# Kernel tuning notes

Hardware: AMD Instinct MI355X
Metric: run time of the kernel (lower is better)

## Reference

```python
import jax, jax.numpy as jnp
import numpy as np

K = 24          # SiFinder.KERNEL_SIZE
SIGMA = 1e-6    # SiFinder.CORR_SIGMA


def setup_inputs() -> dict:
    key = jax.random.key(0)
    k1, k2, k3 = jax.random.split(key, 3)
    H = W = 480
    x_dec = jax.random.normal(k1, (1, 3, H, W), dtype=jnp.float32)
    y_dec = jax.random.normal(k2, (1, 3, H, W), dtype=jnp.float32)
    y = jax.random.normal(k3, (1, 3, H, W), dtype=jnp.float32)
    return {"x_dec": x_dec, "y_dec": y_dec, "y": y}


def _get_x_patches(x_dec):
    # non-overlapping KxK patches, raster order (rows of patches, then cols)
    _, C, H, W = x_dec.shape
    p = x_dec[0].reshape(C, H // K, K, W // K, K)
    return p.transpose(1, 3, 0, 2, 4).reshape(-1, C, K, K)  # (P, C, K, K)


def _conv(img, w):
    # valid cross-correlation, matches F.conv2d
    return jax.lax.conv_general_dilated(
        img, w, window_strides=(1, 1), padding='VALID',
        dimension_numbers=('NCHW', 'OIHW', 'NCHW'))


def _pearson_corr(x_patches, y):
    C = x_patches.shape[1]
    ps = C * K * K  # patch_size
    mean_x = jnp.mean(x_patches, axis=(1, 2, 3))[None, :, None, None]   # (1,P,1,1)
    sum_x2 = jnp.sum(x_patches ** 2, axis=(1, 2, 3))[None, :, None, None]
    ones = jnp.ones((1, C, K, K), y.dtype)
    sum_y = _conv(y, ones)            # (1,1,H',W'); torch builds P identical channels
    xy = _conv(y, x_patches)          # (1,P,H',W')
    numer = xy / ps - mean_x * sum_y / ps
    den_x = sum_x2 / ps - mean_x ** 2
    den_y = _conv(y ** 2, ones) / ps - sum_y ** 2 / ps ** 2
    return (2 * numer + SIGMA) / (jnp.abs(den_x) + jnp.abs(den_y) + SIGMA)


def _forward(x_dec, y_dec, y):
    x_patches = _get_x_patches(x_dec)
    corr = _pearson_corr(x_patches, y_dec)          # (1, P, H', W')
    _, P, Hc, Wc = corr.shape
    idx = jnp.argmax(corr[0].reshape(P, Hc * Wc), axis=-1)
    rows, cols = idx // Wc, idx % Wc
    # roi_align(boxes=[-0.5+c, -0.5+r, ...], out=KxK, sampling_ratio=-1) samples
    # exactly at integer pixel centers -> reduces to an exact patch gather from y.
    C = y.shape[1]
    def take(r, c):
        return jax.lax.dynamic_slice(y[0], (0, r, c), (C, K, K))
    patches = jax.vmap(take)(rows, cols)            # (P, C, K, K)
    # nn.Fold with stride==kernel: stitch non-overlapping patches back to image
    H, W = x_dec.shape[2], x_dec.shape[3]
    img = patches.reshape(H // K, W // K, C, K, K).transpose(2, 0, 3, 1, 4)
    return img.reshape(1, C, H, W)


def reference(x_dec, y_dec, y):
    return _forward(x_dec, y_dec, y)
```

## Files before the change

### kernel.cpp

```cpp
#include <hip/hip_runtime.h>
#include <stdint.h>

#define HW    480
#define KS    24
#define CH    3
#define HO    457
#define NPOS  (HO*HO)
#define NP    400
#define PS    (CH*KS*KS)
#define SIG   1e-6f
#define NSQ   54
#define NMT   13
#define NIY   115
#define NGRP  (NIY*8*4)
#define MAXF  16384
#define RGRID 4096
#define DELTA 4e-3f
#define QS    28.0f
#define IS2   (1.0f/(QS*QS))
#define PB    2608

typedef __attribute__((ext_vector_type(4)))  int  int4v;
typedef __attribute__((ext_vector_type(16))) int  int16v;
typedef unsigned int uint;
typedef unsigned char uchar;
typedef unsigned long long ull;

static __device__ __forceinline__ char q8(float v) {
    float s = rintf(v * QS);
    s = fminf(127.f, fmaxf(-127.f, s));
    return (char)(int)s;
}
static __device__ __forceinline__ uint mono(float f) {
    uint u = __float_as_uint(f);
    return (u & 0x80000000u) ? ~u : (u | 0x80000000u);
}
static __device__ __forceinline__ float unmono(uint u) {
    uint b = (u & 0x80000000u) ? (u & 0x7fffffffu) : ~u;
    return __uint_as_float(b);
}

__global__ void fat1_k(const float* __restrict__ x, const float* __restrict__ yd,
                       float* __restrict__ Wp, char* __restrict__ yq,
                       float* __restrict__ cs, float* __restrict__ cs2) {
    int b = blockIdx.x;
    if (b < 2700) {
        int t = b * 256 + threadIdx.x;
        int p = t / PS, e = t - p * PS;
        int c = e / (KS * KS);
        int r = (e / KS) % KS;
        int w = e % KS;
        int pr = p / 20, pc = p - pr * 20;
        Wp[t] = x[c * HW * HW + (pr * KS + r) * HW + (pc * KS + w)];
    } else if (b < 5400) {
        int t = (b - 2700) * 256 + threadIdx.x;
        yq[t] = q8(yd[t]);
    } else {
        int t = (b - 5400) * 256 + threadIdx.x;
        if (t >= HO * HW) return;
        int i = t / HW, w = t - i * HW;
        float s = 0.f, s2 = 0.f;
        for (int c = 0; c < CH; c++) {
            const float* base = yd + c * HW * HW + i * HW + w;
            for (int dh = 0; dh < KS; dh++) {
                float v = base[dh * HW];
                s += v; s2 += v * v;
            }
        }
        cs[t] = s; cs2[t] = s2;
    }
}

__global__ void fat2_k(const float* __restrict__ Wp,
                       const float* __restrict__ cs, const float* __restrict__ cs2,
                       float* __restrict__ meanX, float* __restrict__ denXa,
                       char* __restrict__ Aq,
                       float* __restrict__ sumY, float* __restrict__ denYa,
                       uint* __restrict__ cnt, ull* __restrict__ best) {
    __shared__ float shs[4], shs2[4];
    int b = blockIdx.x;
    if (b < 400) {
        int p = b;
        if (threadIdx.x == 1) best[p] = 0ull;
        if (b == 0 && threadIdx.x == 2) *cnt = 0u;
        float s = 0.f, s2 = 0.f;
        for (int e = threadIdx.x; e < PS; e += 256) {
            float v = Wp[p * PS + e];
            s += v; s2 += v * v;
        }
        for (int o = 32; o > 0; o >>= 1) { s += __shfl_down(s, o); s2 += __shfl_down(s2, o); }
        int lane = threadIdx.x & 63, wv = threadIdx.x >> 6;
        if (lane == 0) { shs[wv] = s; shs2[wv] = s2; }
        __syncthreads();
        if (threadIdx.x == 0) {
            float S = shs[0] + shs[1] + shs[2] + shs[3];
            float S2 = shs2[0] + shs2[1] + shs2[2] + shs2[3];
            float m = S / (float)PS;
            meanX[p] = m;
            denXa[p] = fabsf(S2 / (float)PS - m * m);
        }
    } else if (b < 3208) {
        int id = (b - 400) * 256 + threadIdx.x;
        int e    = id & 15;
        int lane = (id >> 4) & 63;
        int f    = id >> 10;
        int s    = f % NSQ;
        int mtg  = f / NSQ;
        int kk = s * 32 + (lane >> 5) * 16 + e;
        int p  = mtg * 32 + (lane & 31);
        float v = (p < NP) ? Wp[p * PS + kk] : 0.f;
        Aq[id] = q8(v);
    } else {
        int t = (b - 3208) * 256 + threadIdx.x;
        if (t >= NPOS) return;
        int i = t / HO, j = t - i * HO;
        const float* r  = cs  + i * HW + j;
        const float* r2 = cs2 + i * HW + j;
        float s = 0.f, s2 = 0.f;
        for (int d = 0; d < KS; d++) { s += r[d]; s2 += r2[d]; }
        sumY[t] = s;
        float ips = 1.0f / (float)PS;
        denYa[t] = fabsf(s2 * ips - (s * ips) * (s * ips));
    }
}

static __device__ __forceinline__ void stage_c(uchar* __restrict__ S,
                                               const char* __restrict__ yq,
                                               int c, int i0, int j0, int tid) {
    for (int it = tid; it < 27 * 6; it += 256) {
        int row = it / 6;
        int gb  = (it - row * 6) * 16;
        int yr  = i0 + row;
        int gj  = j0 + gb;
        uint d[6];
        if (yr < HW && gj + 24 <= HW) {
            const uchar* src = (const uchar*)yq + ((size_t)(c * HW + yr)) * HW + gj;
            uint4 a = *(const uint4*)src;
            uint2 bb = *(const uint2*)(src + 16);
            d[0] = a.x; d[1] = a.y; d[2] = a.z; d[3] = a.w; d[4] = bb.x; d[5] = bb.y;
        } else {
            uchar tmp[24];
#pragma unroll
            for (int e = 0; e < 24; e++) {
                int col = gj + e;
                tmp[e] = (yr < HW && col < HW)
                       ? ((const uchar*)yq)[((size_t)(c * HW + yr)) * HW + col] : (uchar)0;
            }
            const uint* tp = (const uint*)tmp;
#pragma unroll
            for (int e = 0; e < 6; e++) d[e] = tp[e];
        }
        int base = row * 96 + gb;
#pragma unroll
        for (int pi = 0; pi < 8; pi++) {
            const int a = pi >> 2;
            const int r = pi & 3;
            uint4 w;
            if (r == 0)
                w = make_uint4(d[a], d[a + 1], d[a + 2], d[a + 3]);
            else
                w = make_uint4((d[a]     >> (8 * r)) | (d[a + 1] << (32 - 8 * r)),
                               (d[a + 1] >> (8 * r)) | (d[a + 2] << (32 - 8 * r)),
                               (d[a + 2] >> (8 * r)) | (d[a + 3] << (32 - 8 * r)),
                               (d[a + 3] >> (8 * r)) | (d[a + 4] << (32 - 8 * r)));
            *(uint4*)&S[pi * PB + base] = w;
        }
    }
}

template<int MT>
static __device__ __forceinline__ void corr1_body(
        const int mt0,
        const char* __restrict__ yq, const char* __restrict__ Aq,
        const float* __restrict__ meanX, const float* __restrict__ denXa,
        const float* __restrict__ sumY, const float* __restrict__ denYa,
        uint* __restrict__ table, uchar* __restrict__ S) {
    const int tid  = threadIdx.x;
    const int lane = tid & 63;
    const int g    = tid >> 6;
    const int n    = lane & 31;
    const int kha  = lane >> 5;
    const int jx   = blockIdx.x;
    const int iy   = blockIdx.y;
    const int j0   = 64 * jx;
    const int i0   = 4 * iy;
    const int i    = i0 + g;

    const int olo[3] = { kha ? 16  : 0,   kha ? 192 : 104, kha ? 296 : 208 };
    const int ohi[3] = { kha ? 96  : 8,   kha ? 200 : 112, kha ? 304 : 288 };

    const uchar* Bt0g = S + ((2 * n) & 7) * PB + ((2 * n) & ~7) + g * 96;
    const uchar* Bt1g = Bt0g + PB;

    const char* Ab0 = Aq + ((size_t)mt0 * NSQ << 10) + lane * 16;
    const char* Ab[2] = { Ab0, Ab0 + ((size_t)NSQ << 10) };

    int16v acc[MT][2];
#pragma unroll
    for (int mt = 0; mt < MT; mt++)
#pragma unroll
        for (int t = 0; t < 2; t++) acc[mt][t] = (int16v)0;

    int4v av[2][MT][3];
#pragma unroll
    for (int mt = 0; mt < MT; mt++)
#pragma unroll
        for (int u = 0; u < 3; u++)
            av[0][mt][u] = *(const int4v*)(Ab[mt] + (u << 10));

#pragma unroll
    for (int c = 0; c < CH; c++) {
        __syncthreads();
        stage_c(S, yq, c, i0, j0, tid);
        __syncthreads();

#pragma unroll
        for (int q = 0; q < 6; q++) {
            const int Q   = c * 6 + q;
            const int cur = Q & 1;
            if (Q < 17) {
#pragma unroll
                for (int mt = 0; mt < MT; mt++)
#pragma unroll
                    for (int u = 0; u < 3; u++)
                        av[cur ^ 1][mt][u] =
                            *(const int4v*)(Ab[mt] + (((Q + 1) * 3 + u) << 10));
            }
            const uchar* Bq0 = Bt0g + 384 * q;
            const uchar* Bq1 = Bt1g + 384 * q;
            uint2 blo[3][2], bhi[3][2];
#pragma unroll
            for (int u = 0; u < 3; u++) {
                blo[u][0] = *(const uint2*)(Bq0 + olo[u]);
                bhi[u][0] = *(const uint2*)(Bq0 + ohi[u]);
                blo[u][1] = *(const uint2*)(Bq1 + olo[u]);
                bhi[u][1] = *(const uint2*)(Bq1 + ohi[u]);
            }
#pragma unroll
            for (int u = 0; u < 3; u++)
#pragma unroll
                for (int t = 0; t < 2; t++) {
                    int4v bv;
                    bv.x = (int)blo[u][t].x; bv.y = (int)blo[u][t].y;
                    bv.z = (int)bhi[u][t].x; bv.w = (int)bhi[u][t].y;
#pragma unroll
                    for (int mt = 0; mt < MT; mt++)
                        acc[mt][t] = __builtin_amdgcn_mfma_i32_32x32x32_i8(
                                         av[cur][mt][u], bv, acc[mt][t], 0, 0, 0);
                }
        }
    }

    const int grp = (iy * 8 + jx) * 4 + g;
    const float c2 = 2.0f / (float)PS;
    const bool iok = i < HO;
    float sYv[2], rDv[2];
#pragma unroll
    for (int t = 0; t < 2; t++) {
        int j = j0 + 2 * n + t;
        bool ok = iok && (j < HO);
        sYv[t] = ok ? sumY[i * HO + j] : 0.f;
        rDv[t] = ok ? denYa[i * HO + j] : 0.f;
    }
    const bool jv0 = iok && (j0 + 2 * n + 0 < HO);
    const bool jv1 = iok && (j0 + 2 * n + 1 < HO);
#pragma unroll
    for (int mt = 0; mt < MT; mt++) {
        const int pbase = (mt0 + mt) * 32;
#pragma unroll
        for (int r = 0; r < 16; r++) {
            int p = pbase + (r & 3) + 8 * (r >> 2) + 4 * kha;
            bool pok = p < NP;
            float mX = pok ? meanX[p] : 0.f;
            float dX = pok ? denXa[p] : 0.f;
            float num[2], den[2];
#pragma unroll
            for (int t = 0; t < 2; t++) {
                bool ok = t ? jv1 : jv0;
                if (ok) {
                    float xy = (float)acc[mt][t][r] * IS2;
                    num[t] = fmaf(-mX, sYv[t], xy) * c2 + SIG;
                    den[t] = dX + rDv[t] + SIG;
                } else {
                    num[t] = -3.0e38f;
                    den[t] = 1.0f;
                }
            }
            bool pick1 = num[1] * den[0] > num[0] * den[1];
            float nn = pick1 ? num[1] : num[0];
            float dd = pick1 ? den[1] : den[0];
            float bu = nn * __builtin_amdgcn_rcpf(dd);
#pragma unroll
            for (int o = 1; o < 32; o <<= 1)
                bu = fmaxf(bu, __shfl_xor(bu, o));
            if (n == 0 && pok) table[p * NGRP + grp] = mono(bu);
        }
    }
}

__launch_bounds__(256, 3)
__global__ void corr1_k(const char* __restrict__ yq, const char* __restrict__ Aq,
                        const float* __restrict__ meanX, const float* __restrict__ denXa,
                        const float* __restrict__ sumY, const float* __restrict__ denYa,
                        uint* __restrict__ table) {
    __shared__ __align__(16) uchar S[8 * PB];
    if (blockIdx.z == 6)
        corr1_body<1>(12, yq, Aq, meanX, denXa, sumY, denYa, table, S);
    else
        corr1_body<2>(2 * blockIdx.z, yq, Aq, meanX, denXa, sumY, denYa, table, S);
}

__global__ void flag_k(const uint* __restrict__ table,
                       uint* __restrict__ flags, uint* __restrict__ cnt) {
    __shared__ uint sm[4];
    __shared__ float sthr;
    int p = blockIdx.x;
    uint m = 0;
    for (int g = threadIdx.x; g < NGRP; g += 256) {
        uint v = table[p * NGRP + g];
        m = v > m ? v : m;
    }
    for (int o = 32; o > 0; o >>= 1) { uint ot = __shfl_down(m, o); m = ot > m ? ot : m; }
    int lane = threadIdx.x & 63, wv = threadIdx.x >> 6;
    if (lane == 0) sm[wv] = m;
    __syncthreads();
    if (threadIdx.x == 0) {
        uint mm = max(max(sm[0], sm[1]), max(sm[2], sm[3]));
        sthr = unmono(mm) - DELTA;
    }
    __syncthreads();
    float thr = sthr;
    for (int g = threadIdx.x; g < NGRP; g += 256) {
        if (unmono(table[p * NGRP + g]) >= thr) {
            uint idx = atomicAdd(cnt, 1u);
            if (idx < MAXF) flags[idx] = (uint)(p * NGRP + g);
        }
    }
}

__launch_bounds__(64)
__global__ void rescore_k(const float* __restrict__ Wp, const float* __restrict__ y_dec,
                          const float* __restrict__ meanX, const float* __restrict__ denXa,
                          const float* __restrict__ sumY, const float* __restrict__ denYa,
                          const uint* __restrict__ flags, const uint* __restrict__ cnt,
                          ull* __restrict__ best) {
    uint nflag = *cnt; if (nflag > MAXF) nflag = MAXF;
    for (uint fb = blockIdx.x; fb < nflag; fb += RGRID) {
        uint f = flags[fb];
        int p = f / NGRP, grp = f - p * NGRP;
        int g = grp & 3, bj = grp >> 2;
        int jx = bj & 7, iy = bj >> 3;
        int i = 4 * iy + g;
        int j = 64 * jx + threadIdx.x;
        ull pk = 0;
        if (i < HO && j < HO) {
            float dot = 0.f;
            const float* wr = Wp + p * PS;
            for (int c = 0; c < CH; c++)
                for (int kh = 0; kh < KS; kh++) {
                    const float* yr = y_dec + ((c * HW) + i + kh) * HW + j;
                    const float* wk = wr + (c * KS + kh) * KS;
#pragma unroll
                    for (int kw = 0; kw < KS; kw++) dot += wk[kw] * yr[kw];
                }
            float corr = (2.0f * (dot - meanX[p] * sumY[i * HO + j]) * (1.0f / (float)PS) + SIG)
                       / (denXa[p] + denYa[i * HO + j] + SIG);
            uint idx = (uint)(i * HO + j);
            pk = ((ull)mono(corr) << 32) | (uint)(~idx);
        }
        for (int o = 32; o > 0; o >>= 1) { ull ot = __shfl_down(pk, o); pk = ot > pk ? ot : pk; }
        if (threadIdx.x == 0) atomicMax(&best[p], pk);
    }
}

__global__ void gather_k(const float* __restrict__ y,
                         const ull* __restrict__ best,
                         float* __restrict__ out) {
    int p = blockIdx.x;
    uint idx = ~((uint)(best[p] & 0xFFFFFFFFull));
    int r = idx / HO, cc = idx - r * HO;
    int pr = p / 20, pc = p - pr * 20;
    for (int e = threadIdx.x; e < PS; e += 256) {
        int c = e / (KS * KS);
        int kh = (e / KS) % KS;
        int kw = e % KS;
        out[c * HW * HW + (pr * KS + kh) * HW + (pc * KS + kw)] =
            y[c * HW * HW + (r + kh) * HW + (cc + kw)];
    }
}

extern "C" void kernel_launch(void* const* d_in, const int* in_sizes, int n_in,
                              void* d_out, int out_size, void* d_ws, size_t ws_size,
                              hipStream_t stream) {
    const float* x_dec = (const float*)d_in[0];
    const float* y_dec = (const float*)d_in[1];
    const float* y     = (const float*)d_in[2];
    float* out = (float*)d_out;

    char* ws = (char*)d_ws;
    size_t off = 0;
    auto carve = [&](size_t bytes) -> void* {
        void* p = ws + off;
        off += (bytes + 255) & ~(size_t)255;
        return p;
    };
    float*  Wp    = (float*)carve((size_t)NP * PS * 4);
    char*   yq    = (char*)carve((size_t)CH * HW * HW);
    char*   Aq    = (char*)carve((size_t)NMT * NSQ * 1024);
    float*  cs    = (float*)carve((size_t)HO * HW * 4);
    float*  cs2   = (float*)carve((size_t)HO * HW * 4);
    float*  sumY  = (float*)carve((size_t)NPOS * 4);
    float*  denYa = (float*)carve((size_t)NPOS * 4);
    float*  meanX = (float*)carve((size_t)NP * 4);
    float*  denXa = (float*)carve((size_t)NP * 4);
    uint*   table = (uint*)carve((size_t)NP * NGRP * 4);
    uint*   flags = (uint*)carve((size_t)MAXF * 4);
    uint*   cnt   = (uint*)carve(256);
    ull*    best  = (ull*)carve((size_t)NP * 8);

    fat1_k<<<6257, 256, 0, stream>>>(x_dec, y_dec, Wp, yq, cs, cs2);
    fat2_k<<<4024, 256, 0, stream>>>(Wp, cs, cs2, meanX, denXa, Aq, sumY, denYa, cnt, best);

    dim3 grid(8, NIY, 7);
    corr1_k<<<grid, 256, 0, stream>>>(yq, Aq, meanX, denXa, sumY, denYa, table);

    flag_k<<<NP, 256, 0, stream>>>(table, flags, cnt);
    rescore_k<<<RGRID, 64, 0, stream>>>(Wp, y_dec, meanX, denXa, sumY, denYa, flags, cnt, best);

    gather_k<<<NP, 256, 0, stream>>>(y, best, out);
}
```

Baseline: 375.1 us.

## Use one M-tile per block and prefetch next channel's global loads

The correlation kernel now gives each block a single 32-patch M-tile instead of two, which moves the grid z-dimension from 7 to 13 and raises the launch-bounds occupancy target from 3 to 4 blocks. Staging of the y input into shared memory is split into a global load into registers and a separate shared-memory write. The next channel's load is issued right after the barrier so it overlaps the MFMA work. In exchange, every y tile is staged into LDS twice as often across blocks, and each block gets less B-fragment reuse per LDS read.

```diff
diff --git a/kernel.cpp b/kernel.cpp
--- a/kernel.cpp
+++ b/kernel.cpp
@@ -124,17 +124,36 @@
     }
 }
 
-static __device__ __forceinline__ void stage_c(uchar* __restrict__ S,
-                                               const char* __restrict__ yq,
-                                               int c, int i0, int j0, int tid) {
-    for (int it = tid; it < 27 * 6; it += 256) {
-        int row = it / 6;
-        int gb  = (it - row * 6) * 16;
-        int yr  = i0 + row;
-        int gj  = j0 + gb;
-        uint d[6];
-        if (yr < HW && gj + 24 <= HW) {
-            const uchar* src = (const uchar*)yq + ((size_t)(c * HW + yr)) * HW + gj;
+__launch_bounds__(256, 4)
+__global__ void corr1_k(const char* __restrict__ yq, const char* __restrict__ Aq,
+                        const float* __restrict__ meanX, const float* __restrict__ denXa,
+                        const float* __restrict__ sumY, const float* __restrict__ denYa,
+                        uint* __restrict__ table) {
+    __shared__ __align__(16) uchar S[8 * PB];
+
+    const int tid  = threadIdx.x;
+    const int lane = tid & 63;
+    const int g    = tid >> 6;
+    const int n    = lane & 31;
+    const int kha  = lane >> 5;
+    const int jx   = blockIdx.x;
+    const int iy   = blockIdx.y;
+    const int mt0  = blockIdx.z;
+    const int j0   = 64 * jx;
+    const int i0   = 4 * iy;
+    const int i    = i0 + g;
+
+    const int  srow = tid / 6;
+    const int  sgb  = (tid - srow * 6) * 16;
+    const bool sact = tid < 27 * 6;
+    const int  syr  = i0 + srow;
+    const int  sgj  = j0 + sgb;
+
+    uint d[6];
+    auto load_c = [&](int c) {
+        if (!sact) return;
+        if (syr < HW && sgj + 24 <= HW) {
+            const uchar* src = (const uchar*)yq + ((size_t)(c * HW + syr)) * HW + sgj;
             uint4 a = *(const uint4*)src;
             uint2 bb = *(const uint2*)(src + 16);
             d[0] = a.x; d[1] = a.y; d[2] = a.z; d[3] = a.w; d[4] = bb.x; d[5] = bb.y;
@@ -142,15 +161,18 @@
             uchar tmp[24];
 #pragma unroll
             for (int e = 0; e < 24; e++) {
-                int col = gj + e;
-                tmp[e] = (yr < HW && col < HW)
-                       ? ((const uchar*)yq)[((size_t)(c * HW + yr)) * HW + col] : (uchar)0;
+                int col = sgj + e;
+                tmp[e] = (syr < HW && col < HW)
+                       ? ((const uchar*)yq)[((size_t)(c * HW + syr)) * HW + col] : (uchar)0;
             }
             const uint* tp = (const uint*)tmp;
 #pragma unroll
             for (int e = 0; e < 6; e++) d[e] = tp[e];
         }
-        int base = row * 96 + gb;
+    };
+    auto write_S = [&]() {
+        if (!sact) return;
+        int base = srow * 96 + sgb;
 #pragma unroll
         for (int pi = 0; pi < 8; pi++) {
             const int a = pi >> 2;
@@ -165,26 +187,7 @@
                                (d[a + 3] >> (8 * r)) | (d[a + 4] << (32 - 8 * r)));
             *(uint4*)&S[pi * PB + base] = w;
         }
-    }
-}
-
-template<int MT>
-static __device__ __forceinline__ void corr1_body(
-        const int mt0,
-        const char* __restrict__ yq, const char* __restrict__ Aq,
-        const float* __restrict__ meanX, const float* __restrict__ denXa,
-        const float* __restrict__ sumY, const float* __restrict__ denYa,
-        uint* __restrict__ table, uchar* __restrict__ S) {
-    const int tid  = threadIdx.x;
-    const int lane = tid & 63;
-    const int g    = tid >> 6;
-    const int n    = lane & 31;
-    const int kha  = lane >> 5;
-    const int jx   = blockIdx.x;
-    const int iy   = blockIdx.y;
-    const int j0   = 64 * jx;
-    const int i0   = 4 * iy;
-    const int i    = i0 + g;
+    };
 
     const int olo[3] = { kha ? 16  : 0,   kha ? 192 : 104, kha ? 296 : 208 };
     const int ohi[3] = { kha ? 96  : 8,   kha ? 200 : 112, kha ? 304 : 288 };
@@ -192,27 +195,24 @@
     const uchar* Bt0g = S + ((2 * n) & 7) * PB + ((2 * n) & ~7) + g * 96;
     const uchar* Bt1g = Bt0g + PB;
 
-    const char* Ab0 = Aq + ((size_t)mt0 * NSQ << 10) + lane * 16;
-    const char* Ab[2] = { Ab0, Ab0 + ((size_t)NSQ << 10) };
-
-    int16v acc[MT][2];
-#pragma unroll
-    for (int mt = 0; mt < MT; mt++)
-#pragma unroll
-        for (int t = 0; t < 2; t++) acc[mt][t] = (int16v)0;
-
-    int4v av[2][MT][3];
-#pragma unroll
-    for (int mt = 0; mt < MT; mt++)
-#pragma unroll
-        for (int u = 0; u < 3; u++)
-            av[0][mt][u] = *(const int4v*)(Ab[mt] + (u << 10));
+    const char* Ab = Aq + ((size_t)mt0 * NSQ << 10) + lane * 16;
+
+    int16v acc[2];
+#pragma unroll
+    for (int t = 0; t < 2; t++) acc[t] = (int16v)0;
+
+    load_c(0);
+    int4v av[2][3];
+#pragma unroll
+    for (int u = 0; u < 3; u++)
+        av[0][u] = *(const int4v*)(Ab + (u << 10));
 
 #pragma unroll
     for (int c = 0; c < CH; c++) {
         __syncthreads();
-        stage_c(S, yq, c, i0, j0, tid);
+        write_S();
         __syncthreads();
+        if (c < CH - 1) load_c(c + 1);
 
 #pragma unroll
         for (int q = 0; q < 6; q++) {
@@ -220,11 +220,8 @@
             const int cur = Q & 1;
             if (Q < 17) {
 #pragma unroll
-                for (int mt = 0; mt < MT; mt++)
-#pragma unroll
-                    for (int u = 0; u < 3; u++)
-                        av[cur ^ 1][mt][u] =
-                            *(const int4v*)(Ab[mt] + (((Q + 1) * 3 + u) << 10));
+                for (int u = 0; u < 3; u++)
+                    av[cur ^ 1][u] = *(const int4v*)(Ab + (((Q + 1) * 3 + u) << 10));
             }
             const uchar* Bq0 = Bt0g + 384 * q;
             const uchar* Bq1 = Bt1g + 384 * q;
@@ -243,10 +240,8 @@
                     int4v bv;
                     bv.x = (int)blo[u][t].x; bv.y = (int)blo[u][t].y;
                     bv.z = (int)bhi[u][t].x; bv.w = (int)bhi[u][t].y;
-#pragma unroll
-                    for (int mt = 0; mt < MT; mt++)
-                        acc[mt][t] = __builtin_amdgcn_mfma_i32_32x32x32_i8(
-                                         av[cur][mt][u], bv, acc[mt][t], 0, 0, 0);
+                    acc[t] = __builtin_amdgcn_mfma_i32_32x32x32_i8(
+                                 av[cur][u], bv, acc[t], 0, 0, 0);
                 }
         }
     }
@@ -264,50 +259,35 @@
     }
     const bool jv0 = iok && (j0 + 2 * n + 0 < HO);
     const bool jv1 = iok && (j0 + 2 * n + 1 < HO);
-#pragma unroll
-    for (int mt = 0; mt < MT; mt++) {
-        const int pbase = (mt0 + mt) * 32;
-#pragma unroll
-        for (int r = 0; r < 16; r++) {
-            int p = pbase + (r & 3) + 8 * (r >> 2) + 4 * kha;
-            bool pok = p < NP;
-            float mX = pok ? meanX[p] : 0.f;
-            float dX = pok ? denXa[p] : 0.f;
-            float num[2], den[2];
-#pragma unroll
-            for (int t = 0; t < 2; t++) {
-                bool ok = t ? jv1 : jv0;
-                if (ok) {
-                    float xy = (float)acc[mt][t][r] * IS2;
-                    num[t] = fmaf(-mX, sYv[t], xy) * c2 + SIG;
-                    den[t] = dX + rDv[t] + SIG;
-                } else {
-                    num[t] = -3.0e38f;
-                    den[t] = 1.0f;
-                }
+    const int pbase = mt0 * 32;
+#pragma unroll
+    for (int r = 0; r < 16; r++) {
+        int p = pbase + (r & 3) + 8 * (r >> 2) + 4 * kha;
+        bool pok = p < NP;
+        float mX = pok ? meanX[p] : 0.f;
+        float dX = pok ? denXa[p] : 0.f;
+        float num[2], den[2];
+#pragma unroll
+        for (int t = 0; t < 2; t++) {
+            bool ok = t ? jv1 : jv0;
+            if (ok) {
+                float xy = (float)acc[t][r] * IS2;
+                num[t] = fmaf(-mX, sYv[t], xy) * c2 + SIG;
+                den[t] = dX + rDv[t] + SIG;
+            } else {
+                num[t] = -3.0e38f;
+                den[t] = 1.0f;
             }
-            bool pick1 = num[1] * den[0] > num[0] * den[1];
-            float nn = pick1 ? num[1] : num[0];
-            float dd = pick1 ? den[1] : den[0];
-            float bu = nn * __builtin_amdgcn_rcpf(dd);
-#pragma unroll
-            for (int o = 1; o < 32; o <<= 1)
-                bu = fmaxf(bu, __shfl_xor(bu, o));
-            if (n == 0 && pok) table[p * NGRP + grp] = mono(bu);
-        }
-    }
-}
-
-__launch_bounds__(256, 3)
-__global__ void corr1_k(const char* __restrict__ yq, const char* __restrict__ Aq,
-                        const float* __restrict__ meanX, const float* __restrict__ denXa,
-                        const float* __restrict__ sumY, const float* __restrict__ denYa,
-                        uint* __restrict__ table) {
-    __shared__ __align__(16) uchar S[8 * PB];
-    if (blockIdx.z == 6)
-        corr1_body<1>(12, yq, Aq, meanX, denXa, sumY, denYa, table, S);
-    else
-        corr1_body<2>(2 * blockIdx.z, yq, Aq, meanX, denXa, sumY, denYa, table, S);
+        }
+        bool pick1 = num[1] * den[0] > num[0] * den[1];
+        float nn = pick1 ? num[1] : num[0];
+        float dd = pick1 ? den[1] : den[0];
+        float bu = nn * __builtin_amdgcn_rcpf(dd);
+#pragma unroll
+        for (int o = 1; o < 32; o <<= 1)
+            bu = fmaxf(bu, __shfl_xor(bu, o));
+        if (n == 0 && pok) table[p * NGRP + grp] = mono(bu);
+    }
 }
 
 __global__ void flag_k(const uint* __restrict__ table,
@@ -421,7 +401,7 @@
     fat1_k<<<6257, 256, 0, stream>>>(x_dec, y_dec, Wp, yq, cs, cs2);
     fat2_k<<<4024, 256, 0, stream>>>(Wp, cs, cs2, meanX, denXa, Aq, sumY, denYa, cnt, best);
 
-    dim3 grid(8, NIY, 7);
+    dim3 grid(8, NIY, NMT);
     corr1_k<<<grid, 256, 0, stream>>>(yq, Aq, meanX, denXa, sumY, denYa, table);
 
     flag_k<<<NP, 256, 0, stream>>>(table, flags, cnt);
```

New measurement: 400.4 us. +6.7%, slower.

## Double-buffer shared-memory staging of int8 image rows across channels

Applied to the files above, without the earlier changes.

Replaces the per-channel synchronous staging of quantized image rows into LDS with a two-buffer pipeline. The next channel's global loads are issued in registers after the first MFMA step, and the shifted copies are written to the alternate buffer partway through the current channel's MFMA loop. This removes one barrier per channel and hides global load latency behind tensor-core work. In exchange LDS use doubles to about 42KB per block, which may reduce occupancy under the launch bound of 3 blocks, and the prefetched data adds register pressure.

```diff
diff --git a/kernel.cpp b/kernel.cpp
--- a/kernel.cpp
+++ b/kernel.cpp
@@ -19,6 +19,7 @@
 #define QS    28.0f
 #define IS2   (1.0f/(QS*QS))
 #define PB    2608
+#define BUFB  (8*PB)
 
 typedef __attribute__((ext_vector_type(4)))  int  int4v;
 typedef __attribute__((ext_vector_type(16))) int  int16v;
@@ -124,50 +125,6 @@
     }
 }
 
-static __device__ __forceinline__ void stage_c(uchar* __restrict__ S,
-                                               const char* __restrict__ yq,
-                                               int c, int i0, int j0, int tid) {
-    for (int it = tid; it < 27 * 6; it += 256) {
-        int row = it / 6;
-        int gb  = (it - row * 6) * 16;
-        int yr  = i0 + row;
-        int gj  = j0 + gb;
-        uint d[6];
-        if (yr < HW && gj + 24 <= HW) {
-            const uchar* src = (const uchar*)yq + ((size_t)(c * HW + yr)) * HW + gj;
-            uint4 a = *(const uint4*)src;
-            uint2 bb = *(const uint2*)(src + 16);
-            d[0] = a.x; d[1] = a.y; d[2] = a.z; d[3] = a.w; d[4] = bb.x; d[5] = bb.y;
-        } else {
-            uchar tmp[24];
-#pragma unroll
-            for (int e = 0; e < 24; e++) {
-                int col = gj + e;
-                tmp[e] = (yr < HW && col < HW)
-                       ? ((const uchar*)yq)[((size_t)(c * HW + yr)) * HW + col] : (uchar)0;
-            }
-            const uint* tp = (const uint*)tmp;
-#pragma unroll
-            for (int e = 0; e < 6; e++) d[e] = tp[e];
-        }
-        int base = row * 96 + gb;
-#pragma unroll
-        for (int pi = 0; pi < 8; pi++) {
-            const int a = pi >> 2;
-            const int r = pi & 3;
-            uint4 w;
-            if (r == 0)
-                w = make_uint4(d[a], d[a + 1], d[a + 2], d[a + 3]);
-            else
-                w = make_uint4((d[a]     >> (8 * r)) | (d[a + 1] << (32 - 8 * r)),
-                               (d[a + 1] >> (8 * r)) | (d[a + 2] << (32 - 8 * r)),
-                               (d[a + 2] >> (8 * r)) | (d[a + 3] << (32 - 8 * r)),
-                               (d[a + 3] >> (8 * r)) | (d[a + 4] << (32 - 8 * r)));
-            *(uint4*)&S[pi * PB + base] = w;
-        }
-    }
-}
-
 template<int MT>
 static __device__ __forceinline__ void corr1_body(
         const int mt0,
@@ -186,11 +143,56 @@
     const int i0   = 4 * iy;
     const int i    = i0 + g;
 
+    const int  srow = tid / 6;
+    const int  sgb  = (tid - srow * 6) * 16;
+    const bool sact = tid < 27 * 6;
+    const int  syr  = i0 + srow;
+    const int  sgj  = j0 + sgb;
+
+    uint d[6];
+    auto load_c = [&](int c) {
+        if (!sact) return;
+        if (syr < HW && sgj + 24 <= HW) {
+            const uchar* src = (const uchar*)yq + ((size_t)(c * HW + syr)) * HW + sgj;
+            uint4 a = *(const uint4*)src;
+            uint2 bb = *(const uint2*)(src + 16);
+            d[0] = a.x; d[1] = a.y; d[2] = a.z; d[3] = a.w; d[4] = bb.x; d[5] = bb.y;
+        } else {
+            uchar tmp[24];
+#pragma unroll
+            for (int e = 0; e < 24; e++) {
+                int col = sgj + e;
+                tmp[e] = (syr < HW && col < HW)
+                       ? ((const uchar*)yq)[((size_t)(c * HW + syr)) * HW + col] : (uchar)0;
+            }
+            const uint* tp = (const uint*)tmp;
+#pragma unroll
+            for (int e = 0; e < 6; e++) d[e] = tp[e];
+        }
+    };
+    auto write_S = [&](uchar* B) {
+        if (!sact) return;
+        int base = srow * 96 + sgb;
+#pragma unroll
+        for (int pi = 0; pi < 8; pi++) {
+            const int a = pi >> 2;
+            const int r = pi & 3;
+            uint4 w;
+            if (r == 0)
+                w = make_uint4(d[a], d[a + 1], d[a + 2], d[a + 3]);
+            else
+                w = make_uint4((d[a]     >> (8 * r)) | (d[a + 1] << (32 - 8 * r)),
+                               (d[a + 1] >> (8 * r)) | (d[a + 2] << (32 - 8 * r)),
+                               (d[a + 2] >> (8 * r)) | (d[a + 3] << (32 - 8 * r)),
+                               (d[a + 3] >> (8 * r)) | (d[a + 4] << (32 - 8 * r)));
+            *(uint4*)&B[pi * PB + base] = w;
+        }
+    };
+
     const int olo[3] = { kha ? 16  : 0,   kha ? 192 : 104, kha ? 296 : 208 };
     const int ohi[3] = { kha ? 96  : 8,   kha ? 200 : 112, kha ? 304 : 288 };
 
-    const uchar* Bt0g = S + ((2 * n) & 7) * PB + ((2 * n) & ~7) + g * 96;
-    const uchar* Bt1g = Bt0g + PB;
+    const int boff = ((2 * n) & 7) * PB + ((2 * n) & ~7) + g * 96;
 
     const char* Ab0 = Aq + ((size_t)mt0 * NSQ << 10) + lane * 16;
     const char* Ab[2] = { Ab0, Ab0 + ((size_t)NSQ << 10) };
@@ -201,23 +203,27 @@
 #pragma unroll
         for (int t = 0; t < 2; t++) acc[mt][t] = (int16v)0;
 
+    load_c(0);
     int4v av[2][MT][3];
 #pragma unroll
     for (int mt = 0; mt < MT; mt++)
 #pragma unroll
         for (int u = 0; u < 3; u++)
             av[0][mt][u] = *(const int4v*)(Ab[mt] + (u << 10));
+    write_S(S);
+    __syncthreads();
 
 #pragma unroll
     for (int c = 0; c < CH; c++) {
-        __syncthreads();
-        stage_c(S, yq, c, i0, j0, tid);
-        __syncthreads();
+        const uchar* Bt0g = S + (c & 1) * BUFB + boff;
+        const uchar* Bt1g = Bt0g + PB;
 
 #pragma unroll
         for (int q = 0; q < 6; q++) {
             const int Q   = c * 6 + q;
             const int cur = Q & 1;
+            if (q == 4 && c < CH - 1)
+                write_S(S + ((c + 1) & 1) * BUFB);
             if (Q < 17) {
 #pragma unroll
                 for (int mt = 0; mt < MT; mt++)
@@ -248,7 +254,10 @@
                         acc[mt][t] = __builtin_amdgcn_mfma_i32_32x32x32_i8(
                                          av[cur][mt][u], bv, acc[mt][t], 0, 0, 0);
                 }
-        }
+            if (q == 0 && c < CH - 1)
+                load_c(c + 1);
+        }
+        if (c < CH - 1) __syncthreads();
     }
 
     const int grp = (iy * 8 + jx) * 4 + g;
@@ -303,7 +312,7 @@
                         const float* __restrict__ meanX, const float* __restrict__ denXa,
                         const float* __restrict__ sumY, const float* __restrict__ denYa,
                         uint* __restrict__ table) {
-    __shared__ __align__(16) uchar S[8 * PB];
+    __shared__ __align__(16) uchar S[2 * BUFB];
     if (blockIdx.z == 6)
         corr1_body<1>(12, yq, Aq, meanX, denXa, sumY, denYa, table, S);
     else
```

Result: no change. 381.5 us (+1.7%).

## Stage all three channels in LDS once and build odd shifts with byte permutes

Applied to the files above, without the earlier changes.

The int8 Y tile for all three channels is now staged into shared memory in a single pass with one barrier, instead of restaging per channel between two barriers each. Only four shifted copies per channel are stored (shifts 0, 2, 4, 6) rather than eight. The odd-shift B operand is rebuilt in registers with v_perm byte shifts from an extra 8-byte LDS load. This removes the per-channel sync stalls and most of the LDS write traffic. In exchange the LDS footprint grows (about 31 KB versus about 21 KB), which may reduce occupancy, and the inner loop gets extra LDS loads and ALU permutes.

```diff
diff --git a/kernel.cpp b/kernel.cpp
--- a/kernel.cpp
+++ b/kernel.cpp
@@ -18,7 +18,9 @@
 #define DELTA 4e-3f
 #define QS    28.0f
 #define IS2   (1.0f/(QS*QS))
-#define PB    2608
+#define PLS   2592
+#define CHS   (4*PLS)
+#define LDSZ  (3*CHS)
 
 typedef __attribute__((ext_vector_type(4)))  int  int4v;
 typedef __attribute__((ext_vector_type(16))) int  int16v;
@@ -124,50 +126,6 @@
     }
 }
 
-static __device__ __forceinline__ void stage_c(uchar* __restrict__ S,
-                                               const char* __restrict__ yq,
-                                               int c, int i0, int j0, int tid) {
-    for (int it = tid; it < 27 * 6; it += 256) {
-        int row = it / 6;
-        int gb  = (it - row * 6) * 16;
-        int yr  = i0 + row;
-        int gj  = j0 + gb;
-        uint d[6];
-        if (yr < HW && gj + 24 <= HW) {
-            const uchar* src = (const uchar*)yq + ((size_t)(c * HW + yr)) * HW + gj;
-            uint4 a = *(const uint4*)src;
-            uint2 bb = *(const uint2*)(src + 16);
-            d[0] = a.x; d[1] = a.y; d[2] = a.z; d[3] = a.w; d[4] = bb.x; d[5] = bb.y;
-        } else {
-            uchar tmp[24];
-#pragma unroll
-            for (int e = 0; e < 24; e++) {
-                int col = gj + e;
-                tmp[e] = (yr < HW && col < HW)
-                       ? ((const uchar*)yq)[((size_t)(c * HW + yr)) * HW + col] : (uchar)0;
-            }
-            const uint* tp = (const uint*)tmp;
-#pragma unroll
-            for (int e = 0; e < 6; e++) d[e] = tp[e];
-        }
-        int base = row * 96 + gb;
-#pragma unroll
-        for (int pi = 0; pi < 8; pi++) {
-            const int a = pi >> 2;
-            const int r = pi & 3;
-            uint4 w;
-            if (r == 0)
-                w = make_uint4(d[a], d[a + 1], d[a + 2], d[a + 3]);
-            else
-                w = make_uint4((d[a]     >> (8 * r)) | (d[a + 1] << (32 - 8 * r)),
-                               (d[a + 1] >> (8 * r)) | (d[a + 2] << (32 - 8 * r)),
-                               (d[a + 2] >> (8 * r)) | (d[a + 3] << (32 - 8 * r)),
-                               (d[a + 3] >> (8 * r)) | (d[a + 4] << (32 - 8 * r)));
-            *(uint4*)&S[pi * PB + base] = w;
-        }
-    }
-}
-
 template<int MT>
 static __device__ __forceinline__ void corr1_body(
         const int mt0,
@@ -186,11 +144,46 @@
     const int i0   = 4 * iy;
     const int i    = i0 + g;
 
+    for (int it = tid; it < 3 * 27 * 6; it += 256) {
+        int ch  = it / 162, rem = it - ch * 162;
+        int row = rem / 6,  gb  = rem - row * 6;
+        int yr  = i0 + row;
+        int gj  = j0 + gb * 16;
+        uint d[6];
+        if (yr < HW && gj + 24 <= HW) {
+            const uchar* src = (const uchar*)yq + ((size_t)(ch * HW + yr)) * HW + gj;
+            uint4 a = *(const uint4*)src;
+            uint2 bb = *(const uint2*)(src + 16);
+            d[0] = a.x; d[1] = a.y; d[2] = a.z; d[3] = a.w; d[4] = bb.x; d[5] = bb.y;
+        } else {
+            uchar tmp[24];
+#pragma unroll
+            for (int e = 0; e < 24; e++) {
+                int col = gj + e;
+                tmp[e] = (yr < HW && col < HW)
+                       ? ((const uchar*)yq)[((size_t)(ch * HW + yr)) * HW + col] : (uchar)0;
+            }
+            const uint* tp = (const uint*)tmp;
+#pragma unroll
+            for (int e = 0; e < 6; e++) d[e] = tp[e];
+        }
+        int base = ch * CHS + row * 96 + gb * 16;
+        uint s0 = (d[0] >> 16) | (d[1] << 16);
+        uint s1 = (d[1] >> 16) | (d[2] << 16);
+        uint s2 = (d[2] >> 16) | (d[3] << 16);
+        uint s3 = (d[3] >> 16) | (d[4] << 16);
+        uint s4 = (d[4] >> 16) | (d[5] << 16);
+        *(uint4*)&S[base]           = make_uint4(d[0], d[1], d[2], d[3]);
+        *(uint4*)&S[base + PLS]     = make_uint4(s0, s1, s2, s3);
+        *(uint4*)&S[base + 2*PLS]   = make_uint4(d[1], d[2], d[3], d[4]);
+        *(uint4*)&S[base + 3*PLS]   = make_uint4(s1, s2, s3, s4);
+    }
+    __syncthreads();
+
     const int olo[3] = { kha ? 16  : 0,   kha ? 192 : 104, kha ? 296 : 208 };
     const int ohi[3] = { kha ? 96  : 8,   kha ? 200 : 112, kha ? 304 : 288 };
 
-    const uchar* Bt0g = S + ((2 * n) & 7) * PB + ((2 * n) & ~7) + g * 96;
-    const uchar* Bt1g = Bt0g + PB;
+    const uchar* Sp = S + (n & 3) * PLS + ((2 * n) & ~7) + g * 96;
 
     const char* Ab0 = Aq + ((size_t)mt0 * NSQ << 10) + lane * 16;
     const char* Ab[2] = { Ab0, Ab0 + ((size_t)NSQ << 10) };
@@ -209,45 +202,37 @@
             av[0][mt][u] = *(const int4v*)(Ab[mt] + (u << 10));
 
 #pragma unroll
-    for (int c = 0; c < CH; c++) {
-        __syncthreads();
-        stage_c(S, yq, c, i0, j0, tid);
-        __syncthreads();
-
-#pragma unroll
-        for (int q = 0; q < 6; q++) {
-            const int Q   = c * 6 + q;
-            const int cur = Q & 1;
-            if (Q < 17) {
-#pragma unroll
-                for (int mt = 0; mt < MT; mt++)
-#pragma unroll
-                    for (int u = 0; u < 3; u++)
-                        av[cur ^ 1][mt][u] =
-                            *(const int4v*)(Ab[mt] + (((Q + 1) * 3 + u) << 10));
+    for (int Q = 0; Q < 18; Q++) {
+        const int cur = Q & 1;
+        if (Q < 17) {
+#pragma unroll
+            for (int mt = 0; mt < MT; mt++)
+#pragma unroll
+                for (int u = 0; u < 3; u++)
+                    av[cur ^ 1][mt][u] =
+                        *(const int4v*)(Ab[mt] + (((Q + 1) * 3 + u) << 10));
+        }
+        const int IQ = (Q / 6) * CHS + (Q % 6) * 384;
+#pragma unroll
+        for (int u = 0; u < 3; u++) {
+            uint2 wl0 = *(const uint2*)(Sp + IQ + olo[u]);
+            uint2 wl1 = *(const uint2*)(Sp + IQ + olo[u] + 8);
+            uint2 wh0 = *(const uint2*)(Sp + IQ + ohi[u]);
+            uint2 wh1 = *(const uint2*)(Sp + IQ + ohi[u] + 8);
+            int4v bv0, bv1;
+            bv0.x = (int)wl0.x; bv0.y = (int)wl0.y;
+            bv0.z = (int)wh0.x; bv0.w = (int)wh0.y;
+            bv1.x = (int)__builtin_amdgcn_perm(wl0.y, wl0.x, 0x04030201u);
+            bv1.y = (int)__builtin_amdgcn_perm(wl1.x, wl0.y, 0x04030201u);
+            bv1.z = (int)__builtin_amdgcn_perm(wh0.y, wh0.x, 0x04030201u);
+            bv1.w = (int)__builtin_amdgcn_perm(wh1.x, wh0.y, 0x04030201u);
+#pragma unroll
+            for (int mt = 0; mt < MT; mt++) {
+                acc[mt][0] = __builtin_amdgcn_mfma_i32_32x32x32_i8(
+                                 av[cur][mt][u], bv0, acc[mt][0], 0, 0, 0);
+                acc[mt][1] = __builtin_amdgcn_mfma_i32_32x32x32_i8(
+                                 av[cur][mt][u], bv1, acc[mt][1], 0, 0, 0);
             }
-            const uchar* Bq0 = Bt0g + 384 * q;
-            const uchar* Bq1 = Bt1g + 384 * q;
-            uint2 blo[3][2], bhi[3][2];
-#pragma unroll
-            for (int u = 0; u < 3; u++) {
-                blo[u][0] = *(const uint2*)(Bq0 + olo[u]);
-                bhi[u][0] = *(const uint2*)(Bq0 + ohi[u]);
-                blo[u][1] = *(const uint2*)(Bq1 + olo[u]);
-                bhi[u][1] = *(const uint2*)(Bq1 + ohi[u]);
-            }
-#pragma unroll
-            for (int u = 0; u < 3; u++)
-#pragma unroll
-                for (int t = 0; t < 2; t++) {
-                    int4v bv;
-                    bv.x = (int)blo[u][t].x; bv.y = (int)blo[u][t].y;
-                    bv.z = (int)bhi[u][t].x; bv.w = (int)bhi[u][t].y;
-#pragma unroll
-                    for (int mt = 0; mt < MT; mt++)
-                        acc[mt][t] = __builtin_amdgcn_mfma_i32_32x32x32_i8(
-                                         av[cur][mt][u], bv, acc[mt][t], 0, 0, 0);
-                }
         }
     }
 
@@ -303,7 +288,7 @@
                         const float* __restrict__ meanX, const float* __restrict__ denXa,
                         const float* __restrict__ sumY, const float* __restrict__ denYa,
                         uint* __restrict__ table) {
-    __shared__ __align__(16) uchar S[8 * PB];
+    __shared__ __align__(16) uchar S[LDSZ];
     if (blockIdx.z == 6)
         corr1_body<1>(12, yq, Aq, meanX, denXa, sumY, denYa, table, S);
     else
```

After: 364.8 us. 1.03x faster.
